# Optimization experiments

Hardware: AMD Instinct MI355X
Metric: run time of the kernel (lower is better)

The kernel has to match this reference:

```python
import jax, jax.numpy as jnp
import numpy as np

B = 64        # number of tasks (sequential steps)
D = 512       # knowledge_representation_dim == understanding_representation_dim
M = 8192      # memory_slots
GAMMA = 0.95  # memory_gamma


def setup_inputs() -> dict:
    key = jax.random.key(0)
    k1, k2, k3, k4 = jax.random.split(key, 4)
    ortho = jax.nn.initializers.orthogonal()
    return {
        "k": jax.random.normal(k1, (B, 1, D), jnp.float32),
        "u": jax.random.normal(k2, (B, 1, D), jnp.float32),
        "memory_knowledge": ortho(k3, (D, M), jnp.float32),
        "memory_understanding": ortho(k4, (D, M), jnp.float32),
        "beta_param": jnp.float32(0.0),
        "memory_gamma": jnp.float32(GAMMA),
    }


def reference(k, u, memory_knowledge, memory_understanding, beta_param, memory_gamma):
    n_slots = memory_knowledge.shape[1]
    slot_ids = jnp.arange(n_slots)
    beta = jax.nn.sigmoid(beta_param)

    def step(carry, xs):
        MK, MU, w_w, w_u, w_lu = carry
        k_task, u_task = xs  # each [1, D]
        # cosine similarity of the task key against every memory column: [1, M]
        sim = (k_task @ MK) / (
            jnp.linalg.norm(k_task, axis=-1, keepdims=True)
            * jnp.linalg.norm(MK, axis=0, keepdims=True)
        )
        w_r = jax.nn.softmax(sim, axis=-1)[0]  # [M]
        # zero out the least-used slot (argmin of usage weights)
        keep = (slot_ids != jnp.argmin(w_u))[None, :]  # [1, M]
        MK = jnp.where(keep, MK, 0.0)
        MU = jnp.where(keep, MU, 0.0)
        # usage / write / least-used weight updates
        w_u = memory_gamma * w_u + w_r + w_w
        w_w = beta * jnp.mean(w_r) + (1.0 - beta) * w_lu  # [M] via broadcast of scalar mean
        w_lu = (slot_ids == jnp.argmin(w_u)).astype(MK.dtype)  # one-hot least-used
        # rank-1 write of understanding, then read refined understanding, then write knowledge
        MU = MU + u_task[0][:, None] * w_w[None, :]  # [D, M]
        u_ref = w_r @ MK.T  # [D] -- read uses MK after zeroing, before its write
        MK = MK + k_task[0][:, None] * w_w[None, :]  # [D, M]
        return (MK, MU, w_w, w_u, w_lu), u_ref

    zeros = jnp.zeros((n_slots,), memory_knowledge.dtype)
    init = (memory_knowledge, memory_understanding, zeros, zeros, zeros)
    _, u_refined = jax.lax.scan(step, init, (k, u))
    return u_refined[:, None, :]  # [B, 1, D]
```

## Files before the change

### kernel.cpp

```cpp
#include <hip/hip_runtime.h>
#include <math.h>

#define BB 64
#define DD 512
#define MM 8192
#define K2T 512
#define K2C 16

typedef unsigned long long u64;

template<int CTRL>
__device__ __forceinline__ float dpp_addf(float x) {
    int y = __builtin_amdgcn_update_dpp(0, __float_as_int(x), CTRL, 0xF, 0xF, true);
    return x + __int_as_float(y);
}
__device__ __forceinline__ float wave_sum64(float x) {
    x = dpp_addf<0x111>(x); x = dpp_addf<0x112>(x); x = dpp_addf<0x114>(x); x = dpp_addf<0x118>(x);
    x = dpp_addf<0x142>(x); x = dpp_addf<0x143>(x);
    return __int_as_float(__builtin_amdgcn_readlane(__float_as_int(x), 63));
}
__device__ __forceinline__ float readlane_f(float v, int l) {
    return __int_as_float(__builtin_amdgcn_readlane(__float_as_int(v), l));
}
template<int CTRL>
__device__ __forceinline__ u64 dpp_min_step(u64 k) {
    unsigned lo = (unsigned)k, hi = (unsigned)(k >> 32);
    unsigned nlo = (unsigned)__builtin_amdgcn_update_dpp((int)0xFFFFFFFFu, (int)lo, CTRL, 0xF, 0xF, false);
    unsigned nhi = (unsigned)__builtin_amdgcn_update_dpp((int)0xFFFFFFFFu, (int)hi, CTRL, 0xF, 0xF, false);
    u64 nk = (((u64)nhi) << 32) | (u64)nlo;
    return nk < k ? nk : k;
}
__device__ __forceinline__ u64 wave_min64_lane63(u64 k) {
    k = dpp_min_step<0x111>(k); k = dpp_min_step<0x112>(k); k = dpp_min_step<0x114>(k);
    k = dpp_min_step<0x118>(k); k = dpp_min_step<0x142>(k); k = dpp_min_step<0x143>(k);
    return k;
}
__device__ __forceinline__ u64 wave_min8(u64 k) {
    k = dpp_min_step<0x111>(k); k = dpp_min_step<0x112>(k); k = dpp_min_step<0x114>(k);
    unsigned lo = (unsigned)__builtin_amdgcn_readlane((int)(unsigned)k, 7);
    unsigned hi = (unsigned)__builtin_amdgcn_readlane((int)(unsigned)(k >> 32), 7);
    return (((u64)hi) << 32) | (u64)lo;
}

struct K0Smem {
    float Ks[BB][129];
    float Gs[BB][BB];
};
struct K1Smem {
    float Ks[64 * 65];
    float Ms[64 * 65];
    float sq[4 * 64];
};
#define KA_SMEM ((sizeof(K0Smem) > sizeof(K1Smem)) ? sizeof(K0Smem) : sizeof(K1Smem))

__global__ __launch_bounds__(256) void ka_gram_s0(const float* __restrict__ K, const float* __restrict__ MK0,
                                                  float* __restrict__ G, float* __restrict__ Pfx,
                                                  float* __restrict__ S0p, float* __restrict__ n2p) {
    __shared__ __align__(16) char blob[KA_SMEM];
    const int tid = threadIdx.x;

    if (blockIdx.x == 0) {
        K0Smem* sm = (K0Smem*)blob;
        const int ti = ((tid >> 4) & 15) << 2;
        const int tj = (tid & 15) << 2;
        float acc[4][4];
        #pragma unroll
        for (int i = 0; i < 4; ++i)
            #pragma unroll
            for (int j = 0; j < 4; ++j) acc[i][j] = 0.f;
        for (int d0 = 0; d0 < DD; d0 += 128) {
            #pragma unroll
            for (int i = 0; i < 32; ++i) {
                int e = i * 256 + tid; int r = e >> 7, c = e & 127;
                sm->Ks[r][c] = K[r * DD + d0 + c];
            }
            __syncthreads();
            for (int dl = 0; dl < 128; ++dl) {
                float rv[4], cv[4];
                #pragma unroll
                for (int i = 0; i < 4; ++i) rv[i] = sm->Ks[ti + i][dl];
                #pragma unroll
                for (int j = 0; j < 4; ++j) cv[j] = sm->Ks[tj + j][dl];
                #pragma unroll
                for (int i = 0; i < 4; ++i)
                    #pragma unroll
                    for (int j = 0; j < 4; ++j) acc[i][j] += rv[i] * cv[j];
            }
            __syncthreads();
        }
        #pragma unroll
        for (int i = 0; i < 4; ++i)
            #pragma unroll
            for (int j = 0; j < 4; ++j) {
                G[(ti + i) * BB + tj + j] = acc[i][j];
                sm->Gs[ti + i][tj + j] = acc[i][j];
            }
        __syncthreads();
        const int s = tid & 63, w = tid >> 6;
        for (int rr = 0; rr < 16; ++rr) {
            int row = w * 16 + rr;
            float x = (s < row) ? sm->Gs[row][s] : 0.f;
            #pragma unroll
            for (int o = 1; o < 64; o <<= 1) {
                float y = __shfl_down(x, o);
                if (s + o < 64) x += y;
            }
            Pfx[row * BB + s] = x;
        }
        return;
    }

    K1Smem* sm = (K1Smem*)blob;
    const int b = blockIdx.x - 1;
    const int lane = tid & 63, w = tid >> 6;
    const int jb = (b & 127) * 64;
    const int by = b >> 7;
    const int dbase = by * 256;
    const int t4 = ((w << 2) | (lane >> 4)) << 2;
    const int jq0 = lane & 15;
    float acc[4][4];
    #pragma unroll
    for (int i = 0; i < 4; ++i)
        #pragma unroll
        for (int q = 0; q < 4; ++q) acc[i][q] = 0.f;
    float sqa = 0.f;
    for (int dt = 0; dt < 4; ++dt) {
        int d0 = dbase + dt * 64;
        #pragma unroll
        for (int i = 0; i < 16; ++i) {
            int e = i * 256 + tid; int r = e >> 6, c = e & 63;
            sm->Ks[r * 65 + c] = K[r * DD + d0 + c];
            float m = MK0[(d0 + r) * MM + jb + c];
            sm->Ms[r * 65 + c] = m;
            sqa += m * m;
        }
        __syncthreads();
        #pragma unroll 4
        for (int dl = 0; dl < 64; ++dl) {
            float kv[4], mv[4];
            #pragma unroll
            for (int i = 0; i < 4; ++i) kv[i] = sm->Ks[(t4 + i) * 65 + dl];
            #pragma unroll
            for (int q = 0; q < 4; ++q) mv[q] = sm->Ms[dl * 65 + jq0 + 16 * q];
            #pragma unroll
            for (int i = 0; i < 4; ++i)
                #pragma unroll
                for (int q = 0; q < 4; ++q) acc[i][q] += kv[i] * mv[q];
        }
        __syncthreads();
    }
    #pragma unroll
    for (int i = 0; i < 4; ++i)
        #pragma unroll
        for (int q = 0; q < 4; ++q)
            S0p[by * BB * MM + (t4 + i) * MM + jb + jq0 + 16 * q] = acc[i][q];
    sm->sq[w * 64 + lane] = sqa;
    __syncthreads();
    if (w == 0) n2p[by * MM + jb + lane] =
        sm->sq[lane] + sm->sq[64 + lane] + sm->sq[128 + lane] + sm->sq[192 + lane];
}

__global__ __launch_bounds__(64) void k1b_ecold(const float* __restrict__ S0p,
                                                const float* __restrict__ G,
                                                const float* __restrict__ Pfx,
                                                const float* __restrict__ n2p,
                                                const float* __restrict__ bp,
                                                float* __restrict__ Ecold,
                                                float* __restrict__ Spart) {
    __shared__ float Pfx0s[BB], invks[BB], k2s[BB];
    int tid = threadIdx.x;
    const int b = blockIdx.x;
    int j = b * 64 + tid;
    {
        float g = G[tid * BB + tid];
        k2s[tid] = g;
        invks[tid] = __builtin_amdgcn_rsqf(g);
        Pfx0s[tid] = Pfx[tid * BB + 0];
    }
    const float beta = 1.f / (1.f + expf(-bp[0]));
    const float cuni = beta / (float)MM;
    float n2c = n2p[j] + n2p[MM + j];
    __syncthreads();
    float pa = S0p[j];
    float pb = S0p[BB * MM + j];
    for (int t = 0; t < BB; ++t) {
        float na = 0.f, nb = 0.f;
        if (t + 1 < BB) {
            na = S0p[(t + 1) * MM + j];
            nb = S0p[(BB + t + 1) * MM + j];
        }
        float s0 = pa + pb;
        float d_ = s0 + cuni * Pfx0s[t];
        float cosv = d_ * invks[t] * __builtin_amdgcn_rsqf(n2c);
        float ee = __expf(cosv);
        Ecold[t * MM + j] = ee;
        float rs = wave_sum64(ee);
        if (tid == 0) Spart[t * 128 + b] = rs;
        n2c = n2c + 2.f * cuni * d_ + cuni * cuni * k2s[t];
        pa = na; pb = nb;
    }
}

struct ScanSmem {
    u64   red[2][8];
    float EtabL[BB * BB];
    float EcTabL[BB * BB];
    float invSL[BB];
    float SL[BB];
    int   endL[BB];
    float invS_bc[2];
};
struct K3Smem {
    float Ws[64 * 65];
    float Msub[64 * 65];
};
#define SMEM_BYTES ((sizeof(ScanSmem) > sizeof(K3Smem)) ? sizeof(ScanSmem) : sizeof(K3Smem))

__global__ __launch_bounds__(512) void k23_scan_u1(const float* __restrict__ Ecold,
                                                   const float* __restrict__ G,
                                                   const float* __restrict__ Pfx,
                                                   const float* __restrict__ Spart,
                                                   const float* __restrict__ bp,
                                                   const float* __restrict__ gp,
                                                   const float* __restrict__ MK0,
                                                   float* __restrict__ Etab_g,
                                                   float* __restrict__ EcTab_g,
                                                   float* __restrict__ Sg,
                                                   float* __restrict__ invSg,
                                                   int*   __restrict__ endTab_g,
                                                   int*   __restrict__ hcolg,
                                                   float* __restrict__ parts) {
    __shared__ __align__(16) char smem_raw[SMEM_BYTES];
    const int tid = threadIdx.x;

    if (blockIdx.x != 0) {
        K3Smem* sm = (K3Smem*)smem_raw;
        const int tile = blockIdx.x - 1;
        const int d0 = (tile & 7) * 64;
        const int by = tile >> 3;
        const bool act = tid < 256;
        const int lane = tid & 63, w = tid >> 6;
        const int t4 = ((w << 2) | (lane >> 4)) << 2;
        const int dq0 = lane & 15;
        float acc[4][4];
        #pragma unroll
        for (int i = 0; i < 4; ++i)
            #pragma unroll
            for (int q = 0; q < 4; ++q) acc[i][q] = 0.f;
        for (int sub = 0; sub < 4; ++sub) {
            int jb = by * 256 + sub * 64;
            if (act) {
                #pragma unroll
                for (int i = 0; i < 16; ++i) {
                    int e = i * 256 + tid; int r = e >> 6, c = e & 63;
                    sm->Ws[r * 65 + c] = Ecold[r * MM + jb + c];
                    sm->Msub[r * 65 + c] = MK0[(d0 + r) * MM + jb + c];
                }
            }
            __syncthreads();
            if (act) {
                #pragma unroll 4
                for (int jl = 0; jl < 64; ++jl) {
                    float wv[4], mv[4];
                    #pragma unroll
                    for (int i = 0; i < 4; ++i) wv[i] = sm->Ws[(t4 + i) * 65 + jl];
                    #pragma unroll
                    for (int q = 0; q < 4; ++q) mv[q] = sm->Msub[(dq0 + 16 * q) * 65 + jl];
                    #pragma unroll
                    for (int i = 0; i < 4; ++i)
                        #pragma unroll
                        for (int q = 0; q < 4; ++q) acc[i][q] += wv[i] * mv[q];
                }
            }
            __syncthreads();
        }
        if (act) {
            #pragma unroll
            for (int i = 0; i < 4; ++i)
                #pragma unroll
                for (int q = 0; q < 4; ++q)
                    parts[(by * 64 + t4 + i) * DD + d0 + dq0 + 16 * q] = acc[i][q];
        }
        return;
    }

    ScanSmem* sm = (ScanSmem*)smem_raw;
    const int lane = tid & 63;
    const int wid = tid >> 6;
    const bool w0 = (wid == 0);

    const float beta  = 1.f / (1.f + expf(-bp[0]));
    const float gamma = gp[0];
    const float cuni  = beta / (float)MM;
    const float omb   = 1.f - beta;

    if (tid < BB) sm->endL[tid] = BB;

    const float4* Ec4 = reinterpret_cast<const float4*>(Ecold);

    float wu[K2C], e0[K2C], e1[K2C], e2[K2C];
    #pragma unroll
    for (int c = 0; c < K2C; ++c) wu[c] = 0.f;
    #pragma unroll
    for (int i = 0; i < K2C / 4; ++i) {
        float4 v = Ec4[i * K2T + tid];
        e0[4 * i + 0] = v.x; e0[4 * i + 1] = v.y; e0[4 * i + 2] = v.z; e0[4 * i + 3] = v.w;
        float4 u = Ec4[(MM / 4) + i * K2T + tid];
        e1[4 * i + 0] = u.x; e1[4 * i + 1] = u.y; e1[4 * i + 2] = u.z; e1[4 * i + 3] = u.w;
    }

    float scold_r = 0.f;
    if (w0) {
        const float4* sp4 = reinterpret_cast<const float4*>(Spart + lane * 128);
        float sc = 0.f;
        #pragma unroll 8
        for (int i = 0; i < 32; ++i) {
            float4 v = sp4[i];
            sc += v.x; sc += v.y; sc += v.z; sc += v.w;
        }
        scold_r = sc;
    }

    float slot_n2 = 0.f, slot_ec = 0.f, wu_hot = 0.f, e_true_c = 0.f;
    int   slot_j = -1;
    bool  slot_act = false;
    float k2_cur = 0.f, S_reg = 0.f, invS_reg = 0.f;

    if (w0) {
        float g0 = G[lane];
        k2_cur = readlane_f(g0, 0);
        S_reg = readlane_f(scold_r, 0);
        invS_reg = __builtin_amdgcn_rcpf(S_reg);
        if (lane == 0) sm->invS_bc[0] = invS_reg;
    }
    __syncthreads();

    auto step = [&](int t, float (&cur)[K2C], float (&ld)[K2C]) {
        float grow_n = 0.f, pfx_n = 0.f, Ssc_n = 0.f, ecpf0 = 0.f;
        if (w0 && t + 1 < BB) {
            if (slot_act) ecpf0 = Ecold[(t + 1) * MM + slot_j];
            grow_n = G[(t + 1) * BB + lane];
            pfx_n  = Pfx[(t + 1) * BB + lane];
            Ssc_n  = readlane_f(scold_r, t + 1);
        }

        int j0; float minval;
        if (t == 0) { j0 = 0; minval = 0.f; }
        else {
            u64 pm = sm->red[t & 1][lane & 7];
            pm = wave_min8(pm);
            j0 = (int)(pm & 0xFFFFFFFFu);
            minval = __uint_as_float((unsigned)(pm >> 32));
        }
        const float cuni_t = (t == 0) ? 0.f : cuni;
        float invS = w0 ? invS_reg : sm->invS_bc[t & 1];

        float latev = 0.f, ecpf_t = 0.f;
        if (w0 && lane == t) {
            latev = Ecold[t * MM + j0];
            if (t + 1 < BB) ecpf_t = Ecold[(t + 1) * MM + j0];
        }
        __builtin_amdgcn_sched_barrier(0);
        if (t + 2 < BB) {
            #pragma unroll
            for (int i = 0; i < K2C / 4; ++i) {
                float4 v = Ec4[(t + 2) * (MM / 4) + i * K2T + tid];
                ld[4 * i + 0] = v.x; ld[4 * i + 1] = v.y; ld[4 * i + 2] = v.z; ld[4 * i + 3] = v.w;
            }
        }
        __builtin_amdgcn_sched_barrier(0);

        bool fresh = false;
        if (w0) {
            u64 sup = __ballot(slot_act && (slot_j == j0));
            const bool has_sup = (sup != 0ull);
            const int  ssup = has_sup ? (int)__builtin_ctzll(sup) : 0;

            if (slot_act) {
                float ww = cuni + ((t >= 2 && lane == t - 1) ? omb : 0.f);
                wu_hot = fmaf(gamma, wu_hot, fmaf(e_true_c, invS, ww));
            }
            float trans_wu = readlane_f(wu_hot, ssup);
            float trans_E  = readlane_f(e_true_c, ssup);

            if (lane == t) {
                slot_j = j0;
                float ww0 = cuni + ((t >= 1) ? omb : 0.f);
                slot_n2 = ww0 * ww0 * k2_cur;
                slot_act = true;
                if (has_sup) wu_hot = trans_wu;
                fresh = !has_sup;
            }
            if (has_sup) {
                if (lane == ssup) slot_act = false;
                if (lane == t) sm->endL[ssup] = t;
            }

            float etl = e_true_c, ecl = slot_ec;
            if (lane == t) { ecl = latev; etl = has_sup ? trans_E : latev; }
            sm->EtabL[t * BB + lane]  = etl;
            sm->EcTabL[t * BB + lane] = ecl;
            if (lane == 0) { sm->invSL[t] = invS; sm->SL[t] = S_reg; }

            if (fresh) wu_hot = fmaf(gamma, minval, fmaf(latev, invS, cuni_t));

            if (t + 1 < BB) {
                float d_ = cuni * pfx_n;
                if (lane >= 1) d_ += omb * grow_n;
                float k2n   = readlane_f(grow_n, t + 1);
                float invkn = __builtin_amdgcn_rsqf(k2n);
                float ecpf  = (lane == t) ? ecpf_t : ecpf0;
                float myDelta = 0.f;
                float e_n = 0.f;
                if (slot_act) {
                    e_n = __expf(d_ * invkn * __builtin_amdgcn_rsqf(slot_n2));
                    myDelta = e_n - ecpf;
                    slot_n2 = slot_n2 + 2.f * cuni * d_ + cuni * cuni * k2n;
                }
                float S_next = Ssc_n + wave_sum64(myDelta);
                float invS_next = __builtin_amdgcn_rcpf(S_next);
                if (lane == 0) sm->invS_bc[(t + 1) & 1] = invS_next;
                if (slot_act) slot_ec = ecpf;
                e_true_c = e_n;
                k2_cur = k2n;
                S_reg = S_next; invS_reg = invS_next;
            }
        }

        float vmin = 0.f; int jmin = 0;
        #pragma unroll
        for (int i = 0; i < 4; ++i) {
            #pragma unroll
            for (int q = 0; q < 4; ++q) {
                int c = i * 4 + q;
                float wun = fmaf(gamma, wu[c], fmaf(cur[c], invS, cuni_t));
                wu[c] = wun;
                int j = i * 2048 + (tid << 2) + q;
                if (c == 0) { vmin = wun; jmin = j; }
                else if (wun < vmin) { vmin = wun; jmin = j; }
            }
        }
        u64 key = (((u64)__float_as_uint(vmin)) << 32) | (unsigned)jmin;

        if (((j0 >> 2) & (K2T - 1)) == tid) {
            int cj = ((j0 >> 11) << 2) | (j0 & 3);
            #pragma unroll
            for (int c = 0; c < K2C; ++c) if (c == cj) wu[c] = __builtin_inff();
        }

        if (w0) {
            u64 skey = (slot_act && !fresh)
                     ? ((((u64)__float_as_uint(wu_hot)) << 32) | (unsigned)slot_j) : ~0ull;
            key = skey < key ? skey : key;
        }
        key = wave_min64_lane63(key);
        if (lane == 63) sm->red[(t + 1) & 1][wid] = key;

        asm volatile("s_waitcnt lgkmcnt(0)" ::: "memory");
        __builtin_amdgcn_s_barrier();
        asm volatile("" ::: "memory");
    };

    #pragma unroll 1
    for (int th = 0; th < 63; th += 3) {
        step(th + 0, e0, e2);
        step(th + 1, e1, e0);
        step(th + 2, e2, e1);
    }
    step(63, e0, e2);

    for (int i = tid; i < BB * BB; i += K2T) {
        Etab_g[i]  = sm->EtabL[i];
        EcTab_g[i] = sm->EcTabL[i];
    }
    if (tid < BB) {
        Sg[tid] = sm->SL[tid];
        invSg[tid] = sm->invSL[tid];
        endTab_g[tid] = sm->endL[tid];
    }
    if (w0) hcolg[lane] = slot_j;
}

__global__ __launch_bounds__(512) void k4_final(const float* __restrict__ parts,
                                                const float* __restrict__ K,
                                                const float* __restrict__ Etab,
                                                const float* __restrict__ EcTab,
                                                const int*   __restrict__ endTab,
                                                const float* __restrict__ Sg,
                                                const float* __restrict__ invSg,
                                                const float* __restrict__ MK0,
                                                const int*   __restrict__ hcolg,
                                                const float* __restrict__ bp,
                                                float* __restrict__ out) {
    __shared__ float Arow[BB];
    __shared__ float Drow[BB];
    __shared__ int hcs[BB];
    int t = blockIdx.x, d = threadIdx.x;
    if (d < BB) {
        hcs[d] = hcolg[d];
        const float beta = 1.f / (1.f + expf(-bp[0]));
        const float cuni = beta / (float)MM;
        const float omb  = 1.f - beta;
        int s = d;
        float Ev = Etab[t * BB + s];
        int endv = endTab[s];
        bool act = (s <= t) && (t < endv);
        float S = Sg[t], invS = invSg[t];
        float ev = act ? Ev : 0.f;
        float x = ev;
        #pragma unroll
        for (int o = 1; o < 64; o <<= 1) {
            float y = __shfl_down(x, o);
            if (s + o < 64) x += y;
        }
        float suf = x - ev;
        float arow = 0.f;
        if (s < t) {
            float Qe = S - suf;
            arow = cuni * Qe;
            if (s >= 1 && act) arow += omb * Ev;
            arow *= invS;
        }
        Arow[s] = arow;
        Drow[s] = act ? (-invS * EcTab[t * BB + s]) : 0.f;
    }
    __syncthreads();
    float isv = invSg[t];
    float s1 = 0.f;
    #pragma unroll
    for (int p = 0; p < 32; ++p) s1 += parts[(p * 64 + t) * DD + d];
    float s2 = 0.f;
    for (int i = 0; i < BB; ++i) s2 += Drow[i] * MK0[d * MM + hcs[i]];
    float s3 = 0.f;
    for (int i = 0; i < BB; ++i) s3 += Arow[i] * K[i * DD + d];
    out[t * DD + d] = isv * s1 + s2 + s3;
}

extern "C" void kernel_launch(void* const* d_in, const int* in_sizes, int n_in,
                              void* d_out, int out_size, void* d_ws, size_t ws_size,
                              hipStream_t stream) {
    const float* K   = (const float*)d_in[0];
    const float* MK0 = (const float*)d_in[2];
    const float* bp  = (const float*)d_in[4];
    const float* gp  = (const float*)d_in[5];

    float* ws    = (float*)d_ws;
    float* G     = ws;
    float* Pfx   = G + 4096;
    float* S0p   = Pfx + 4096;
    float* n2p   = S0p + 1048576;
    float* Ecold = n2p + 16384;
    float* Spart = Ecold + 524288;
    float* Etab  = Spart + 8192;
    float* EcTab = Etab + 4096;
    float* Sarr  = EcTab + 4096;
    float* invS  = Sarr + 64;
    float* parts = invS + 64;
    int*   hcol  = (int*)(parts + 1048576);
    int*   endT  = hcol + 64;
    float* out   = (float*)d_out;

    ka_gram_s0  <<<257, 256, 0, stream>>>(K, MK0, G, Pfx, S0p, n2p);
    k1b_ecold   <<<128, 64, 0, stream>>>(S0p, G, Pfx, n2p, bp, Ecold, Spart);
    k23_scan_u1 <<<257, 512, 0, stream>>>(Ecold, G, Pfx, Spart, bp, gp, MK0,
                                          Etab, EcTab, Sarr, invS, endT, hcol, parts);
    k4_final    <<<64, 512, 0, stream>>>(parts, K, Etab, EcTab, endT, Sarr, invS, MK0, hcol, bp, out);
}
```

Baseline: 244.3 us.

## Share Ecold tile across two D-halves per block and pre-gather hot MK columns

The GEMM blocks in the fused scan kernel now use all 512 threads. Each block computes two 64-wide D tiles that share one staged Ecold tile, so the grid drops from 257 to 129 blocks and Ecold traffic into shared memory is halved. A new gather kernel copies the 64 hot MK0 columns into a contiguous buffer, so the final kernel reads coalesced rows instead of strided column gathers. The costs are one extra kernel launch and a larger shared-memory footprint per block, which may reduce occupancy.

```diff
diff --git a/kernel.cpp b/kernel.cpp
--- a/kernel.cpp
+++ b/kernel.cpp
@@ -210,11 +210,12 @@
     int   endL[BB];
     float invS_bc[2];
 };
-struct K3Smem {
+struct K3Smem2 {
     float Ws[64 * 65];
-    float Msub[64 * 65];
+    float MsubA[64 * 65];
+    float MsubB[64 * 65];
 };
-#define SMEM_BYTES ((sizeof(ScanSmem) > sizeof(K3Smem)) ? sizeof(ScanSmem) : sizeof(K3Smem))
+#define SMEM_BYTES ((sizeof(ScanSmem) > sizeof(K3Smem2)) ? sizeof(ScanSmem) : sizeof(K3Smem2))
 
 __global__ __launch_bounds__(512) void k23_scan_u1(const float* __restrict__ Ecold,
                                                    const float* __restrict__ G,
@@ -234,14 +235,16 @@
     const int tid = threadIdx.x;
 
     if (blockIdx.x != 0) {
-        K3Smem* sm = (K3Smem*)smem_raw;
-        const int tile = blockIdx.x - 1;
-        const int d0 = (tile & 7) * 64;
-        const int by = tile >> 3;
-        const bool act = tid < 256;
-        const int lane = tid & 63, w = tid >> 6;
+        K3Smem2* sm = (K3Smem2*)smem_raw;
+        const int p = blockIdx.x - 1;
+        const int by = p >> 2;
+        const int half = tid >> 8;
+        const int g = tid & 255;
+        const int d0 = (p & 3) * 128 + half * 64;
+        const int lane = g & 63, w = g >> 6;
         const int t4 = ((w << 2) | (lane >> 4)) << 2;
         const int dq0 = lane & 15;
+        float* Msub = half ? sm->MsubB : sm->MsubA;
         float acc[4][4];
         #pragma unroll
         for (int i = 0; i < 4; ++i)
@@ -249,38 +252,40 @@
             for (int q = 0; q < 4; ++q) acc[i][q] = 0.f;
         for (int sub = 0; sub < 4; ++sub) {
             int jb = by * 256 + sub * 64;
-            if (act) {
+            if (half == 0) {
                 #pragma unroll
                 for (int i = 0; i < 16; ++i) {
-                    int e = i * 256 + tid; int r = e >> 6, c = e & 63;
+                    int e = i * 256 + g; int r = e >> 6, c = e & 63;
                     sm->Ws[r * 65 + c] = Ecold[r * MM + jb + c];
-                    sm->Msub[r * 65 + c] = MK0[(d0 + r) * MM + jb + c];
+                    sm->MsubA[r * 65 + c] = MK0[(d0 + r) * MM + jb + c];
                 }
+            } else {
+                #pragma unroll
+                for (int i = 0; i < 16; ++i) {
+                    int e = i * 256 + g; int r = e >> 6, c = e & 63;
+                    sm->MsubB[r * 65 + c] = MK0[(d0 + r) * MM + jb + c];
+                }
             }
             __syncthreads();
-            if (act) {
-                #pragma unroll 4
-                for (int jl = 0; jl < 64; ++jl) {
-                    float wv[4], mv[4];
+            #pragma unroll 4
+            for (int jl = 0; jl < 64; ++jl) {
+                float wv[4], mv[4];
+                #pragma unroll
+                for (int i = 0; i < 4; ++i) wv[i] = sm->Ws[(t4 + i) * 65 + jl];
+                #pragma unroll
+                for (int q = 0; q < 4; ++q) mv[q] = Msub[(dq0 + 16 * q) * 65 + jl];
+                #pragma unroll
+                for (int i = 0; i < 4; ++i)
                     #pragma unroll
-                    for (int i = 0; i < 4; ++i) wv[i] = sm->Ws[(t4 + i) * 65 + jl];
-                    #pragma unroll
-                    for (int q = 0; q < 4; ++q) mv[q] = sm->Msub[(dq0 + 16 * q) * 65 + jl];
-                    #pragma unroll
-                    for (int i = 0; i < 4; ++i)
-                        #pragma unroll
-                        for (int q = 0; q < 4; ++q) acc[i][q] += wv[i] * mv[q];
-                }
+                    for (int q = 0; q < 4; ++q) acc[i][q] += wv[i] * mv[q];
             }
             __syncthreads();
         }
-        if (act) {
-            #pragma unroll
-            for (int i = 0; i < 4; ++i)
-                #pragma unroll
-                for (int q = 0; q < 4; ++q)
-                    parts[(by * 64 + t4 + i) * DD + d0 + dq0 + 16 * q] = acc[i][q];
-        }
+        #pragma unroll
+        for (int i = 0; i < 4; ++i)
+            #pragma unroll
+            for (int q = 0; q < 4; ++q)
+                parts[(by * 64 + t4 + i) * DD + d0 + dq0 + 16 * q] = acc[i][q];
         return;
     }
 
@@ -481,6 +486,13 @@
     if (w0) hcolg[lane] = slot_j;
 }
 
+__global__ __launch_bounds__(512) void k3b_gather(const float* __restrict__ MK0, const int* __restrict__ hcolg,
+                                                  float* __restrict__ MKhot) {
+    int i = blockIdx.x, d = threadIdx.x;
+    int h = hcolg[i];
+    MKhot[i * DD + d] = MK0[d * MM + h];
+}
+
 __global__ __launch_bounds__(512) void k4_final(const float* __restrict__ parts,
                                                 const float* __restrict__ K,
                                                 const float* __restrict__ Etab,
@@ -488,16 +500,13 @@
                                                 const int*   __restrict__ endTab,
                                                 const float* __restrict__ Sg,
                                                 const float* __restrict__ invSg,
-                                                const float* __restrict__ MK0,
-                                                const int*   __restrict__ hcolg,
+                                                const float* __restrict__ MKhot,
                                                 const float* __restrict__ bp,
                                                 float* __restrict__ out) {
     __shared__ float Arow[BB];
     __shared__ float Drow[BB];
-    __shared__ int hcs[BB];
     int t = blockIdx.x, d = threadIdx.x;
     if (d < BB) {
-        hcs[d] = hcolg[d];
         const float beta = 1.f / (1.f + expf(-bp[0]));
         const float cuni = beta / (float)MM;
         const float omb  = 1.f - beta;
@@ -530,7 +539,7 @@
     #pragma unroll
     for (int p = 0; p < 32; ++p) s1 += parts[(p * 64 + t) * DD + d];
     float s2 = 0.f;
-    for (int i = 0; i < BB; ++i) s2 += Drow[i] * MK0[d * MM + hcs[i]];
+    for (int i = 0; i < BB; ++i) s2 += Drow[i] * MKhot[i * DD + d];
     float s3 = 0.f;
     for (int i = 0; i < BB; ++i) s3 += Arow[i] * K[i * DD + d];
     out[t * DD + d] = isv * s1 + s2 + s3;
@@ -555,14 +564,16 @@
     float* EcTab = Etab + 4096;
     float* Sarr  = EcTab + 4096;
     float* invS  = Sarr + 64;
-    float* parts = invS + 64;
+    float* MKhot = invS + 64;
+    float* parts = MKhot + 32768;
     int*   hcol  = (int*)(parts + 1048576);
     int*   endT  = hcol + 64;
     float* out   = (float*)d_out;
 
     ka_gram_s0  <<<257, 256, 0, stream>>>(K, MK0, G, Pfx, S0p, n2p);
     k1b_ecold   <<<128, 64, 0, stream>>>(S0p, G, Pfx, n2p, bp, Ecold, Spart);
-    k23_scan_u1 <<<257, 512, 0, stream>>>(Ecold, G, Pfx, Spart, bp, gp, MK0,
+    k23_scan_u1 <<<129, 512, 0, stream>>>(Ecold, G, Pfx, Spart, bp, gp, MK0,
                                           Etab, EcTab, Sarr, invS, endT, hcol, parts);
-    k4_final    <<<64, 512, 0, stream>>>(parts, K, Etab, EcTab, endT, Sarr, invS, MK0, hcol, bp, out);
-}
+    k3b_gather  <<<64, 512, 0, stream>>>(MK0, hcol, MKhot);
+    k4_final    <<<64, 512, 0, stream>>>(parts, K, Etab, EcTab, endT, Sarr, invS, MKhot, bp, out);
+}
```

New measurement: 225.3 us. 1.08x faster.
